# Kernel tuning notes

Hardware: AMD Instinct MI355X
Metric: run time of the kernel (lower is better)

## Reference

```python
import jax, jax.numpy as jnp
import numpy as np

H = 512   # hidden_size
E = 512   # choice embedding dim (== hidden in the dummy init)
B = 256   # batch
T = 64    # arg sequence length
V = 10000 # number of choices


def setup_inputs() -> dict:
    key = jax.random.key(0)
    ks = jax.random.split(key, 10)
    s = 0.05
    return {
        "init_state": jax.random.normal(ks[0], (B, H), jnp.float32),
        "choice_embed": jax.random.normal(ks[1], (V, E), jnp.float32),
        "arg_seq": jax.random.randint(ks[2], (B, T), 0, V, jnp.int64),
        # flax LSTMCell equivalent: fused gate weights (order i, f, g, o)
        "Wx": jax.random.normal(ks[3], (E, 4 * H), jnp.float32) * s,
        "Wh": jax.random.normal(ks[4], (H, 4 * H), jnp.float32) * s,
        "b": jnp.zeros((4 * H,), jnp.float32),
        # MLP step-score head: concat(H, E) -> 256 -> 1
        "W1": jax.random.normal(ks[5], (H + E, 256), jnp.float32) * s,
        "b1": jnp.zeros((256,), jnp.float32),
        "W2": jax.random.normal(ks[6], (256, 1), jnp.float32) * s,
        "b2": jnp.zeros((1,), jnp.float32),
    }


def _forward(init_state, choice_embed, arg_seq, Wx, Wh, b, W1, b1, W2, b2):
    # initial carry: zeros + init_state, for both c and h
    c0 = init_state
    h0 = init_state
    x_seq = choice_embed[arg_seq]            # [B, T, E] embedding gather
    xs = jnp.swapaxes(x_seq, 0, 1)           # [T, B, E] for scan

    def step(carry, x):
        c, h = carry
        gates = x @ Wx + h @ Wh + b          # [B, 4H]
        i, f, g, o = jnp.split(gates, 4, axis=-1)
        i = jax.nn.sigmoid(i)
        f = jax.nn.sigmoid(f)
        g = jnp.tanh(g)
        o = jax.nn.sigmoid(o)
        c2 = f * c + i * g
        h2 = o * jnp.tanh(c2)
        return (c2, h2), h2

    _, hs = jax.lax.scan(step, (c0, h0), xs)  # hs: [T, B, H]
    hs = jnp.swapaxes(hs, 0, 1)               # [B, T, H]
    # state fed to the score head at step t is the hidden BEFORE consuming x_t
    state = jnp.concatenate((h0[:, None, :], hs[:, :-1, :]), axis=1)  # [B, T, H]
    state = state.reshape(-1, H)               # [B*T, H]

    feat = jnp.concatenate((state, x_seq.reshape(-1, E)), axis=-1)    # [B*T, H+E]
    hid = jax.nn.relu(feat @ W1 + b1)
    score = hid @ W2 + b2                      # [B*T, 1]
    step_scores = score.reshape(-1, T)         # [B, T]
    return jnp.sum(step_scores, axis=-1, keepdims=True)  # [B, 1]


def reference(init_state, choice_embed, arg_seq, Wx, Wh, b, W1, b1, W2, b2):
    return _forward(init_state, choice_embed, arg_seq, Wx, Wh, b, W1, b1, W2, b2)
```

## Files before the change

### kernel.cpp

```cpp
#include <hip/hip_runtime.h>
#include <hip/hip_bf16.h>
#include <math.h>

#define H   512
#define E   512
#define B_  256
#define T_  64
#define G4  2048
#define C1  256
#define BT  16384

#define SPIN_CAP (1 << 22)

typedef __attribute__((ext_vector_type(8))) short  short8;
typedef __attribute__((ext_vector_type(4))) float  f32x4;
typedef __attribute__((ext_vector_type(4))) int    i32x4;
typedef __attribute__((ext_vector_type(4))) unsigned short ushort4v;
typedef unsigned short ushort;
typedef unsigned long long u64;

#define PITCH_US 544

#define BAR_LGKM() asm volatile("s_waitcnt lgkmcnt(0)\n\ts_barrier" ::: "memory")
#define BAR_ALL()  asm volatile("s_waitcnt vmcnt(0) lgkmcnt(0)\n\ts_barrier" ::: "memory")
#define BAR()      asm volatile("s_barrier" ::: "memory")

__device__ __forceinline__ ushort f2bf(float x) {
    unsigned u = __builtin_bit_cast(unsigned, x);
    unsigned r = (u + 0x7FFFu + ((u >> 16) & 1u)) >> 16;
    return (ushort)r;
}
__device__ __forceinline__ float fast_sig(float x) {
    return __builtin_amdgcn_rcpf(1.f + __expf(-x));
}
__device__ __forceinline__ float fast_tanh(float x) {
    return 1.f - 2.f * __builtin_amdgcn_rcpf(1.f + __expf(2.f * x));
}

#define LOAD4_SC0(v0,v1,v2,v3,p0,p1,p2,p3) \
  asm volatile("global_load_dwordx4 %0, %4, off sc0\n\t" \
               "global_load_dwordx4 %1, %5, off sc0\n\t" \
               "global_load_dwordx4 %2, %6, off sc0\n\t" \
               "global_load_dwordx4 %3, %7, off sc0\n\t" \
               "s_waitcnt vmcnt(0)" \
               : "=&v"(v0), "=&v"(v1), "=&v"(v2), "=&v"(v3) \
               : "v"(p0), "v"(p1), "v"(p2), "v"(p3) : "memory")
#define LOAD4_SC01(v0,v1,v2,v3,p0,p1,p2,p3) \
  asm volatile("global_load_dwordx4 %0, %4, off sc0 sc1\n\t" \
               "global_load_dwordx4 %1, %5, off sc0 sc1\n\t" \
               "global_load_dwordx4 %2, %6, off sc0 sc1\n\t" \
               "global_load_dwordx4 %3, %7, off sc0 sc1\n\t" \
               "s_waitcnt vmcnt(0)" \
               : "=&v"(v0), "=&v"(v1), "=&v"(v2), "=&v"(v3) \
               : "v"(p0), "v"(p1), "v"(p2), "v"(p3) : "memory")

__global__ __launch_bounds__(256) void transpose_cast(
    const float* __restrict__ in, ushort* __restrict__ out, int K, int N)
{
    __shared__ float t[32][33];
    const int k0 = blockIdx.y * 32, n0 = blockIdx.x * 32;
    const int tr = threadIdx.x >> 3;
    const int tc = (threadIdx.x & 7) * 4;
    float4 v = *(const float4*)(in + (size_t)(k0 + tr) * N + n0 + tc);
    t[tr][tc + 0] = v.x; t[tr][tc + 1] = v.y; t[tr][tc + 2] = v.z; t[tr][tc + 3] = v.w;
    __syncthreads();
    ushort4v o = { f2bf(t[tc + 0][tr]), f2bf(t[tc + 1][tr]),
                   f2bf(t[tc + 2][tr]), f2bf(t[tc + 3][tr]) };
    *(ushort4v*)(out + (size_t)(n0 + tr) * K + k0 + tc) = o;
}

__global__ __launch_bounds__(128) void gather_embed_bf16(
    const float* __restrict__ emb, const int* __restrict__ idx,
    ushort* __restrict__ X)
{
    const int r = blockIdx.x;
    const int v = idx[r];
    const int c = threadIdx.x * 4;
    float4 f = *(const float4*)(emb + (size_t)v * E + c);
    ushort4v o = { f2bf(f.x), f2bf(f.y), f2bf(f.z), f2bf(f.w) };
    *(ushort4v*)(X + (size_t)r * E + c) = o;
}

__global__ __launch_bounds__(128) void init_prep(
    const float* __restrict__ init, ushort* __restrict__ h0,
    ushort* __restrict__ S)
{
    const int r = blockIdx.x;
    const int c = threadIdx.x * 4;
    float4 f = *(const float4*)(init + (size_t)r * H + c);
    ushort4v o = { f2bf(f.x), f2bf(f.y), f2bf(f.z), f2bf(f.w) };
    *(ushort4v*)(h0 + (size_t)r * H + c) = o;
    *(ushort4v*)(S + ((size_t)r * T_) * H + c) = o;
}

__global__ __launch_bounds__(256) void zero_buf(int* p, int n) {
    int i = blockIdx.x * 256 + threadIdx.x;
    if (i < n) p[i] = 0;
}

__global__ __launch_bounds__(256, 1) void lstm_fused_main(
    const ushort* __restrict__ WhT, const ushort* __restrict__ WxT,
    const ushort* __restrict__ Xbf, const float* __restrict__ bg,
    const float*  __restrict__ init_state, const ushort* __restrict__ h0,
    ushort* __restrict__ pp0, ushort* __restrict__ pp1,
    ushort* __restrict__ S, int* __restrict__ xcd_tbl, int* __restrict__ flags)
{
    __shared__ __align__(16) ushort hsh[16 * PITCH_US];
    __shared__ __align__(16) ushort xsh[2][16 * PITCH_US];
    __shared__ int exl[256];

    const int tid  = threadIdx.x;
    const int wave = tid >> 6, lane = tid & 63;
    const int quad = lane >> 4, l16 = lane & 15;

    int xcd;
    asm volatile("s_getreg_b32 %0, hwreg(HW_REG_XCC_ID)" : "=s"(xcd));
    if (tid == 0)
        __hip_atomic_store(&xcd_tbl[blockIdx.x], (xcd & 7) + 1,
                           __ATOMIC_RELAXED, __HIP_MEMORY_SCOPE_AGENT);
    if (wave == 0) {
        for (int it = 0; it < SPIN_CAP; ++it) {
            int miss = 0;
#pragma unroll
            for (int j = 0; j < 4; ++j) {
                int i = lane + j * 64;
                int v = __hip_atomic_load(&xcd_tbl[i], __ATOMIC_RELAXED,
                                          __HIP_MEMORY_SCOPE_AGENT);
                exl[i] = (v == 0) ? 0 : (v - 1);
                if (v == 0) miss = 1;
            }
            if (!__any(miss)) break;
            __builtin_amdgcn_s_sleep(4);
        }
    }
    BAR_LGKM();

    int g = 0, m = 0, loc = 0;
    {
        int cntx[8] = {0,0,0,0,0,0,0,0};
        for (int i = 0; i < 256; ++i) cntx[exl[i] & 7]++;
        int take[8], base[8], tA = 0;
        for (int x = 0; x < 8; ++x) {
            int tk = cntx[x] >> 4;
            if (tA + tk > 16) tk = 16 - tA;
            take[x] = tk; base[x] = tA; tA += tk;
        }
        int rc[8] = {0,0,0,0,0,0,0,0}, lc = 0;
        for (int i = 0; i < 256; ++i) {
            int x = exl[i] & 7, r = rc[x]++;
            if ((r >> 4) < take[x]) {
                if (i == (int)blockIdx.x) { g = base[x] + (r >> 4); m = r & 15; loc = 1; }
            } else {
                if (i == (int)blockIdx.x) { g = tA + (lc >> 4); m = lc & 15; loc = 0; }
                lc++;
            }
        }
    }

    const int n0   = g * 16;
    const int jw   = m * 32 + wave * 8;
    const int koff = quad * 8;
    const int ccol = jw + (quad & 1) * 4;
    const int myrow = n0 + l16;

    short8 af[2][16], ax[2][16];
#pragma unroll
    for (int mf = 0; mf < 2; ++mf) {
        const int gate = mf * 2 + (l16 >> 3);
        const size_t rowoff = (size_t)(gate * 512 + jw + (l16 & 7)) * 512 + koff;
        const ushort* bh = WhT + rowoff;
        const ushort* bx = WxT + rowoff;
#pragma unroll
        for (int kk = 0; kk < 16; ++kk) {
            af[mf][kk] = *(const short8*)(bh + kk * 32);
            ax[mf][kk] = *(const short8*)(bx + kk * 32);
        }
    }

    float bgi[4], bgf[4], bgg[4], bgo[4];
#pragma unroll
    for (int r = 0; r < 4; ++r) {
        bgi[r] = bg[ccol + r];
        bgf[r] = bg[512 + ccol + r];
        bgg[r] = bg[1024 + ccol + r];
        bgo[r] = bg[1536 + ccol + r];
    }

    float c[4];
    {
        const float* ip = init_state + (size_t)myrow * H + ccol;
#pragma unroll
        for (int r = 0; r < 4; ++r) c[r] = ip[r];
    }

    int gr[4], gc[4], lo[4];
#pragma unroll
    for (int j = 0; j < 4; ++j) {
        int lin = tid + j * 256;
        gr[j] = lin >> 6; gc[j] = lin & 63;
        int kk = gc[j] >> 2, q = gc[j] & 3;
        lo[j] = kk * PITCH_US + (q * 16 + gr[j]) * 8 + q * 8;
    }

#pragma unroll
    for (int j = 0; j < 4; ++j) {
        i32x4 v = *(const i32x4*)(Xbf + ((size_t)(n0 + gr[j]) * T_) * H + gc[j] * 8);
        *(i32x4*)&xsh[0][lo[j]] = v;
    }
    BAR_LGKM();

    int* gfl = flags + g * 64;
    const int frag_off = lane * 8 + quad * 8;

    for (int t = 0; t < T_ - 1; ++t) {
        i32x4 xv0, xv1, xv2, xv3;
        const int have_x = (t + 1 < T_ - 1);
        if (have_x) {
            xv0 = *(const i32x4*)(Xbf + ((size_t)(n0 + gr[0]) * T_ + t + 1) * H + gc[0] * 8);
            xv1 = *(const i32x4*)(Xbf + ((size_t)(n0 + gr[1]) * T_ + t + 1) * H + gc[1] * 8);
            xv2 = *(const i32x4*)(Xbf + ((size_t)(n0 + gr[2]) * T_ + t + 1) * H + gc[2] * 8);
            xv3 = *(const i32x4*)(Xbf + ((size_t)(n0 + gr[3]) * T_ + t + 1) * H + gc[3] * 8);
        }

        f32x4 ax0 = {}, ax1 = {};
        {
            const ushort* xb = xsh[t & 1];
#pragma unroll
            for (int kk = 0; kk < 16; ++kk) {
                short8 b = *(const short8*)&xb[kk * PITCH_US + frag_off];
                ax0 = __builtin_amdgcn_mfma_f32_16x16x32_bf16(ax[0][kk], b, ax0, 0, 0, 0);
                ax1 = __builtin_amdgcn_mfma_f32_16x16x32_bf16(ax[1][kk], b, ax1, 0, 0, 0);
            }
        }

        if (t > 0) {
            if (wave == 0) {
                const int* fp = gfl + lane;
                for (int it = 0; it < SPIN_CAP; ++it) {
                    int v = (lane < 16)
                        ? __hip_atomic_load(fp, __ATOMIC_RELAXED,
                                            __HIP_MEMORY_SCOPE_AGENT)
                        : 0x7fffffff;
                    if (__all(v >= t)) break;
                    __builtin_amdgcn_s_sleep(1);
                }
            }
            BAR();
        }

        {
            const ushort* hin = (t == 0) ? h0 : ((t & 1) ? pp0 : pp1);
            const ushort* p0 = hin + (size_t)(n0 + gr[0]) * H + gc[0] * 8;
            const ushort* p1 = hin + (size_t)(n0 + gr[1]) * H + gc[1] * 8;
            const ushort* p2 = hin + (size_t)(n0 + gr[2]) * H + gc[2] * 8;
            const ushort* p3 = hin + (size_t)(n0 + gr[3]) * H + gc[3] * 8;
            i32x4 v0, v1, v2, v3;
            if (loc) { LOAD4_SC0(v0, v1, v2, v3, p0, p1, p2, p3); }
            else     { LOAD4_SC01(v0, v1, v2, v3, p0, p1, p2, p3); }
            *(i32x4*)&hsh[lo[0]] = v0;
            *(i32x4*)&hsh[lo[1]] = v1;
            *(i32x4*)&hsh[lo[2]] = v2;
            *(i32x4*)&hsh[lo[3]] = v3;
        }
        BAR_LGKM();

        f32x4 a0 = {}, a1 = {};
#pragma unroll
        for (int kk = 0; kk < 16; ++kk) {
            short8 b = *(const short8*)&hsh[kk * PITCH_US + frag_off];
            a0 = __builtin_amdgcn_mfma_f32_16x16x32_bf16(af[0][kk], b, a0, 0, 0, 0);
            a1 = __builtin_amdgcn_mfma_f32_16x16x32_bf16(af[1][kk], b, a1, 0, 0, 0);
        }

        if (have_x) {
            ushort* xb = xsh[(t + 1) & 1];
            *(i32x4*)&xb[lo[0]] = xv0;
            *(i32x4*)&xb[lo[1]] = xv1;
            *(i32x4*)&xb[lo[2]] = xv2;
            *(i32x4*)&xb[lo[3]] = xv3;
        }

        float hv[4];
#pragma unroll
        for (int r = 0; r < 4; ++r) {
            float v0 = a0[r] + ax0[r], v1 = a1[r] + ax1[r];
            float p0 = __shfl_xor(v0, 32, 64);
            float p1 = __shfl_xor(v1, 32, 64);
            float iv = (quad < 2) ? v0 : p0;
            float fv = (quad < 2) ? p0 : v0;
            float gv = (quad < 2) ? v1 : p1;
            float ov = (quad < 2) ? p1 : v1;
            iv = fast_sig(iv + bgi[r]);
            fv = fast_sig(fv + bgf[r]);
            gv = fast_tanh(gv + bgg[r]);
            ov = fast_sig(ov + bgo[r]);
            float cn = fv * c[r] + iv * gv;
            c[r] = cn;
            hv[r] = ov * fast_tanh(cn);
        }
        if (quad < 2) {
            ushort4v o4 = { f2bf(hv[0]), f2bf(hv[1]), f2bf(hv[2]), f2bf(hv[3]) };
            ushort* hout = (t & 1) ? pp1 : pp0;
            u64* hp = (u64*)(hout + (size_t)myrow * H + ccol);
            if (loc) *hp = __builtin_bit_cast(u64, o4);
            else __hip_atomic_store(hp, __builtin_bit_cast(u64, o4),
                                    __ATOMIC_RELAXED, __HIP_MEMORY_SCOPE_AGENT);
            *(ushort4v*)(S + ((size_t)myrow * T_ + (t + 1)) * H + ccol) = o4;
        }

        BAR_ALL();
        if (tid == 0)
            __hip_atomic_store(gfl + m, t + 1,
                               __ATOMIC_RELAXED, __HIP_MEMORY_SCOPE_AGENT);
    }
}

__global__ __launch_bounds__(256) void gemm_score(
    const ushort* __restrict__ Sm, const ushort* __restrict__ Xbf,
    const ushort* __restrict__ W1T,
    const float* __restrict__ b1, const float* __restrict__ W2,
    float* __restrict__ scores)
{
    const int tid  = threadIdx.x;
    const int wave = tid >> 6, lane = tid & 63;
    const int quad = lane >> 4, l16 = lane & 15;
    const int m0 = blockIdx.y * 128 + wave * 32;
    const int n0 = blockIdx.x * 64;
    const int koff = quad * 8;

    f32x4 acc[2][4] = {};

    for (int src = 0; src < 2; ++src) {
        const ushort* A  = src ? Xbf : Sm;
        const ushort* Bm = W1T + src * 512;
        const ushort* a0p = A + (size_t)(m0 + l16) * H + koff;
        const ushort* a1p = A + (size_t)(m0 + 16 + l16) * H + koff;
        const ushort* bp  = Bm + (size_t)(n0 + l16) * 1024 + koff;
        for (int kk = 0; kk < H; kk += 32) {
            short8 a0 = *(const short8*)(a0p + kk);
            short8 a1 = *(const short8*)(a1p + kk);
#pragma unroll
            for (int nf = 0; nf < 4; ++nf) {
                short8 b = *(const short8*)(bp + (size_t)nf * 16 * 1024 + kk);
                acc[0][nf] = __builtin_amdgcn_mfma_f32_16x16x32_bf16(a0, b, acc[0][nf], 0, 0, 0);
                acc[1][nf] = __builtin_amdgcn_mfma_f32_16x16x32_bf16(a1, b, acc[1][nf], 0, 0, 0);
            }
        }
    }

    float w2v[4], b1v[4];
#pragma unroll
    for (int nf = 0; nf < 4; ++nf) {
        const int col = n0 + nf * 16 + l16;
        w2v[nf] = W2[col];
        b1v[nf] = b1[col];
    }

#pragma unroll
    for (int mf = 0; mf < 2; ++mf) {
#pragma unroll
        for (int r = 0; r < 4; ++r) {
            float p = 0.f;
#pragma unroll
            for (int nf = 0; nf < 4; ++nf)
                p += fmaxf(acc[mf][nf][r] + b1v[nf], 0.f) * w2v[nf];
            p += __shfl_xor(p, 1, 64);
            p += __shfl_xor(p, 2, 64);
            p += __shfl_xor(p, 4, 64);
            p += __shfl_xor(p, 8, 64);
            if (l16 == 0)
                atomicAdd(&scores[m0 + mf * 16 + quad * 4 + r], p);
        }
    }
}

__global__ __launch_bounds__(64) void reduce_scores(
    const float* __restrict__ scores, const float* __restrict__ b2,
    float* __restrict__ out)
{
    const int b    = blockIdx.x;
    const int lane = threadIdx.x;
    float s = scores[(size_t)b * T_ + lane] + b2[0];
#pragma unroll
    for (int off = 32; off; off >>= 1) s += __shfl_xor(s, off, 64);
    if (lane == 0) out[b] = s;
}

extern "C" void kernel_launch(void* const* d_in, const int* in_sizes, int n_in,
                              void* d_out, int out_size, void* d_ws, size_t ws_size,
                              hipStream_t stream)
{
    const float* init_state = (const float*)d_in[0];
    const float* choice_emb = (const float*)d_in[1];
    const int*   arg_seq    = (const int*)  d_in[2];
    const float* Wx         = (const float*)d_in[3];
    const float* Wh         = (const float*)d_in[4];
    const float* bg         = (const float*)d_in[5];
    const float* W1         = (const float*)d_in[6];
    const float* b1         = (const float*)d_in[7];
    const float* W2         = (const float*)d_in[8];
    const float* b2         = (const float*)d_in[9];
    float* out = (float*)d_out;

    ushort* WxT = (ushort*)d_ws;
    ushort* WhT = WxT + 1048576;
    ushort* W1T = WhT + 1048576;
    ushort* Xbf = W1T + 262144;
    ushort* S   = Xbf + 8388608;
    ushort* h0  = S   + 8388608;
    ushort* pp0 = h0  + 131072;
    ushort* pp1 = pp0 + 131072;
    float*  scores  = (float*)(pp1 + 131072);
    int*    xcd_tbl = (int*)(scores + BT);
    int*    flags   = xcd_tbl + 256;

    zero_buf<<<70, 256, 0, stream>>>((int*)scores, BT + 256 + 1024);

    transpose_cast<<<dim3(G4 / 32, E / 32), 256, 0, stream>>>(Wx, WxT, E, G4);
    transpose_cast<<<dim3(G4 / 32, H / 32), 256, 0, stream>>>(Wh, WhT, H, G4);
    transpose_cast<<<dim3(C1 / 32, 1024 / 32), 256, 0, stream>>>(W1, W1T, 1024, C1);

    gather_embed_bf16<<<BT, 128, 0, stream>>>(choice_emb, arg_seq, Xbf);
    init_prep<<<B_, 128, 0, stream>>>(init_state, h0, S);

    lstm_fused_main<<<256, 256, 0, stream>>>(
        WhT, WxT, Xbf, bg, init_state, h0, pp0, pp1, S, xcd_tbl, flags);

    gemm_score<<<dim3(C1 / 64, BT / 128), 256, 0, stream>>>(
        S, Xbf, W1T, b1, W2, scores);
    reduce_scores<<<B_, 64, 0, stream>>>(scores, b2, out);
}
```

Measured before the change: 394.6 us.

## Replace per-block flag array with atomic counter sync, relayout LDS, merge weight prep

Result: faster. 386.2 us (-2.1%).

```diff
diff --git a/kernel.cpp b/kernel.cpp
--- a/kernel.cpp
+++ b/kernel.cpp
@@ -19,11 +19,10 @@
 typedef unsigned short ushort;
 typedef unsigned long long u64;
 
-#define PITCH_US 544
+#define PITCH_US 520
 
 #define BAR_LGKM() asm volatile("s_waitcnt lgkmcnt(0)\n\ts_barrier" ::: "memory")
 #define BAR_ALL()  asm volatile("s_waitcnt vmcnt(0) lgkmcnt(0)\n\ts_barrier" ::: "memory")
-#define BAR()      asm volatile("s_barrier" ::: "memory")
 
 __device__ __forceinline__ ushort f2bf(float x) {
     unsigned u = __builtin_bit_cast(unsigned, x);
@@ -54,11 +53,17 @@
                : "=&v"(v0), "=&v"(v1), "=&v"(v2), "=&v"(v3) \
                : "v"(p0), "v"(p1), "v"(p2), "v"(p3) : "memory")
 
-__global__ __launch_bounds__(256) void transpose_cast(
-    const float* __restrict__ in, ushort* __restrict__ out, int K, int N)
+__global__ __launch_bounds__(256) void prep_weights(
+    const float* __restrict__ Wx, const float* __restrict__ Wh,
+    const float* __restrict__ W1,
+    ushort* __restrict__ WxT, ushort* __restrict__ WhT, ushort* __restrict__ W1T)
 {
     __shared__ float t[32][33];
-    const int k0 = blockIdx.y * 32, n0 = blockIdx.x * 32;
+    int bx = blockIdx.x;
+    const float* in; ushort* out; int K, N, k0, n0;
+    if (bx < 1024)       { in = Wx; out = WxT; K = 512;  N = 2048; k0 = (bx >> 6) * 32; n0 = (bx & 63) * 32; }
+    else if (bx < 2048)  { bx -= 1024; in = Wh; out = WhT; K = 512;  N = 2048; k0 = (bx >> 6) * 32; n0 = (bx & 63) * 32; }
+    else                 { bx -= 2048; in = W1; out = W1T; K = 1024; N = 256;  k0 = (bx >> 3) * 32; n0 = (bx & 7) * 32; }
     const int tr = threadIdx.x >> 3;
     const int tc = (threadIdx.x & 7) * 4;
     float4 v = *(const float4*)(in + (size_t)(k0 + tr) * N + n0 + tc);
@@ -103,7 +108,7 @@
     const ushort* __restrict__ Xbf, const float* __restrict__ bg,
     const float*  __restrict__ init_state, const ushort* __restrict__ h0,
     ushort* __restrict__ pp0, ushort* __restrict__ pp1,
-    ushort* __restrict__ S, int* __restrict__ xcd_tbl, int* __restrict__ flags)
+    ushort* __restrict__ S, int* __restrict__ xcd_tbl, int* __restrict__ cnts)
 {
     __shared__ __align__(16) ushort hsh[16 * PITCH_US];
     __shared__ __align__(16) ushort xsh[2][16 * PITCH_US];
@@ -198,8 +203,7 @@
     for (int j = 0; j < 4; ++j) {
         int lin = tid + j * 256;
         gr[j] = lin >> 6; gc[j] = lin & 63;
-        int kk = gc[j] >> 2, q = gc[j] & 3;
-        lo[j] = kk * PITCH_US + (q * 16 + gr[j]) * 8 + q * 8;
+        lo[j] = gr[j] * PITCH_US + gc[j] * 8;
     }
 
 #pragma unroll
@@ -209,8 +213,8 @@
     }
     BAR_LGKM();
 
-    int* gfl = flags + g * 64;
-    const int frag_off = lane * 8 + quad * 8;
+    int* cnt = cnts + g * 32;
+    const int frag_base = l16 * PITCH_US + quad * 8;
 
     for (int t = 0; t < T_ - 1; ++t) {
         i32x4 xv0, xv1, xv2, xv3;
@@ -227,25 +231,19 @@
             const ushort* xb = xsh[t & 1];
 #pragma unroll
             for (int kk = 0; kk < 16; ++kk) {
-                short8 b = *(const short8*)&xb[kk * PITCH_US + frag_off];
+                short8 b = *(const short8*)&xb[frag_base + kk * 32];
                 ax0 = __builtin_amdgcn_mfma_f32_16x16x32_bf16(ax[0][kk], b, ax0, 0, 0, 0);
                 ax1 = __builtin_amdgcn_mfma_f32_16x16x32_bf16(ax[1][kk], b, ax1, 0, 0, 0);
             }
         }
 
         if (t > 0) {
-            if (wave == 0) {
-                const int* fp = gfl + lane;
-                for (int it = 0; it < SPIN_CAP; ++it) {
-                    int v = (lane < 16)
-                        ? __hip_atomic_load(fp, __ATOMIC_RELAXED,
-                                            __HIP_MEMORY_SCOPE_AGENT)
-                        : 0x7fffffff;
-                    if (__all(v >= t)) break;
-                    __builtin_amdgcn_s_sleep(1);
-                }
+            const int tgt = t << 4;
+            for (int it = 0; it < SPIN_CAP; ++it) {
+                if (__hip_atomic_load(cnt, __ATOMIC_RELAXED,
+                                      __HIP_MEMORY_SCOPE_AGENT) >= tgt) break;
+                __builtin_amdgcn_s_sleep(1);
             }
-            BAR();
         }
 
         {
@@ -267,7 +265,7 @@
         f32x4 a0 = {}, a1 = {};
 #pragma unroll
         for (int kk = 0; kk < 16; ++kk) {
-            short8 b = *(const short8*)&hsh[kk * PITCH_US + frag_off];
+            short8 b = *(const short8*)&hsh[frag_base + kk * 32];
             a0 = __builtin_amdgcn_mfma_f32_16x16x32_bf16(af[0][kk], b, a0, 0, 0, 0);
             a1 = __builtin_amdgcn_mfma_f32_16x16x32_bf16(af[1][kk], b, a1, 0, 0, 0);
         }
@@ -298,20 +296,21 @@
             c[r] = cn;
             hv[r] = ov * fast_tanh(cn);
         }
+
+        ushort4v o4 = { f2bf(hv[0]), f2bf(hv[1]), f2bf(hv[2]), f2bf(hv[3]) };
+        ushort* hout = (t & 1) ? pp1 : pp0;
         if (quad < 2) {
-            ushort4v o4 = { f2bf(hv[0]), f2bf(hv[1]), f2bf(hv[2]), f2bf(hv[3]) };
-            ushort* hout = (t & 1) ? pp1 : pp0;
             u64* hp = (u64*)(hout + (size_t)myrow * H + ccol);
             if (loc) *hp = __builtin_bit_cast(u64, o4);
             else __hip_atomic_store(hp, __builtin_bit_cast(u64, o4),
                                     __ATOMIC_RELAXED, __HIP_MEMORY_SCOPE_AGENT);
+        }
+
+        BAR_ALL();
+        if (tid == 0) atomicAdd(cnt, 1);
+
+        if (quad < 2)
             *(ushort4v*)(S + ((size_t)myrow * T_ + (t + 1)) * H + ccol) = o4;
-        }
-
-        BAR_ALL();
-        if (tid == 0)
-            __hip_atomic_store(gfl + m, t + 1,
-                               __ATOMIC_RELAXED, __HIP_MEMORY_SCOPE_AGENT);
     }
 }
 
@@ -412,19 +411,17 @@
     ushort* pp1 = pp0 + 131072;
     float*  scores  = (float*)(pp1 + 131072);
     int*    xcd_tbl = (int*)(scores + BT);
-    int*    flags   = xcd_tbl + 256;
-
-    zero_buf<<<70, 256, 0, stream>>>((int*)scores, BT + 256 + 1024);
-
-    transpose_cast<<<dim3(G4 / 32, E / 32), 256, 0, stream>>>(Wx, WxT, E, G4);
-    transpose_cast<<<dim3(G4 / 32, H / 32), 256, 0, stream>>>(Wh, WhT, H, G4);
-    transpose_cast<<<dim3(C1 / 32, 1024 / 32), 256, 0, stream>>>(W1, W1T, 1024, C1);
+    int*    cnts    = xcd_tbl + 256;
+
+    zero_buf<<<70, 256, 0, stream>>>((int*)scores, BT + 256 + 512);
+
+    prep_weights<<<2304, 256, 0, stream>>>(Wx, Wh, W1, WxT, WhT, W1T);
 
     gather_embed_bf16<<<BT, 128, 0, stream>>>(choice_emb, arg_seq, Xbf);
     init_prep<<<B_, 128, 0, stream>>>(init_state, h0, S);
 
     lstm_fused_main<<<256, 256, 0, stream>>>(
-        WhT, WxT, Xbf, bg, init_state, h0, pp0, pp1, S, xcd_tbl, flags);
+        WhT, WxT, Xbf, bg, init_state, h0, pp0, pp1, S, xcd_tbl, cnts);
 
     gemm_score<<<dim3(C1 / 64, BT / 128), 256, 0, stream>>>(
         S, Xbf, W1T, b1, W2, scores);
```
